# Kernel optimization log

Measured on AMD Instinct MI355X. Metric: run time of the kernel, lower is better.

Reference implementation:

```python
import jax, jax.numpy as jnp
import numpy as np

B, S, D = 8, 2048, 512

def setup_inputs() -> dict:
    key = jax.random.key(0)
    ks = jax.random.split(key, 9)
    scale = 1.0 / np.sqrt(D)
    q = jax.random.normal(ks[0], (B, S, D), dtype=jnp.float32)
    k = jax.random.normal(ks[1], (B, S, D), dtype=jnp.float32)
    v = jax.random.normal(ks[2], (B, S, D), dtype=jnp.float32)
    # causal mask, broadcast over batch: True = attend
    mask = jnp.tril(jnp.ones((S, S), dtype=bool))[None, :, :]
    Wq = jax.random.normal(ks[3], (D, D), dtype=jnp.float32) * scale
    bq = jax.random.normal(ks[4], (D,), dtype=jnp.float32) * scale
    Wk = jax.random.normal(ks[5], (D, D), dtype=jnp.float32) * scale
    bk = jax.random.normal(ks[6], (D,), dtype=jnp.float32) * scale
    Wv = jax.random.normal(ks[7], (D, D), dtype=jnp.float32) * scale
    bv = jax.random.normal(ks[8], (D,), dtype=jnp.float32) * scale
    return {"q": q, "k": k, "v": v, "mask": mask,
            "Wq": Wq, "bq": bq, "Wk": Wk, "bk": bk, "Wv": Wv, "bv": bv}

def reference(q, k, v, mask, Wq, bq, Wk, bk, Wv, bv):
    # torch nn.Linear: x @ W^T + b
    Q = jnp.einsum('bsd,ed->bse', q, Wq) + bq
    K = jnp.einsum('bsd,ed->bse', k, Wk) + bk
    V = jnp.einsum('bsd,ed->bse', v, Wv) + bv
    scores = jnp.einsum('bqd,bkd->bqk', Q, K) / jnp.sqrt(jnp.float32(D))
    scores = jnp.where(mask, scores, jnp.float32(-1e9))
    prob = jax.nn.softmax(scores, axis=-1)
    out = jnp.einsum('bqk,bkd->bqd', prob, V)
    return out
```

## Files before the change

### kernel.cpp

```cpp
#include <hip/hip_runtime.h>
#include <stdint.h>
#include <stddef.h>
#include <math.h>

typedef _Float16 half8 __attribute__((ext_vector_type(8)));
typedef float f32x4 __attribute__((ext_vector_type(4)));

#define SCALE_QK 0.04419417382415922f

__device__ __forceinline__ void gload16(const void* g, void* lds) {
  __builtin_amdgcn_global_load_lds(
      (const __attribute__((address_space(1))) void*)g,
      (__attribute__((address_space(3))) void*)lds,
      16, 0, 0);
}

template<bool A_F32>
__device__ __forceinline__ void run_kloop(const void* Arow0, const _Float16* Brow0,
                                          int lda, int ldb, int kIters,
                                          _Float16* As0, _Float16* As1,
                                          _Float16* Bs0, _Float16* Bs1,
                                          f32x4 (&acc)[4][4])
{
  const int tid  = threadIdx.x;
  const int lane = tid & 63;
  const int w    = tid >> 6;
  const int wm   = w >> 1, wn = w & 1;
  const int srow = tid >> 3;
  const int sg   = tid & 7;
  const int swz  = sg ^ (srow & 7);
  const int fr   = lane & 15;
  const int fq   = lane >> 4;
  const int fx   = lane & 7;

  f32x4 preF[8];

  auto loadAreg = [&](int it) {
    const float* A = (const float*)Arow0;
    const int k0 = it * 64;
    #pragma unroll
    for (int i = 0; i < 4; ++i) {
      const float* src = A + (size_t)(i*32 + srow) * lda + (k0 + sg*8);
      preF[2*i]   = *(const f32x4*)src;
      preF[2*i+1] = *(const f32x4*)(src + 4);
    }
  };
  auto writeA = [&](_Float16* dst) {
    #pragma unroll
    for (int i = 0; i < 4; ++i) {
      f32x4 x = preF[2*i], y = preF[2*i+1];
      half8 h;
      h[0]=(_Float16)x[0]; h[1]=(_Float16)x[1]; h[2]=(_Float16)x[2]; h[3]=(_Float16)x[3];
      h[4]=(_Float16)y[0]; h[5]=(_Float16)y[1]; h[6]=(_Float16)y[2]; h[7]=(_Float16)y[3];
      *(half8*)(dst + (i*32 + srow)*64 + swz*8) = h;
    }
  };
  auto gloadA = [&](int it, _Float16* dst) {
    const _Float16* A = (const _Float16*)Arow0;
    const int k0 = it * 64;
    #pragma unroll
    for (int i = 0; i < 4; ++i)
      gload16(A + (size_t)(i*32 + srow) * lda + (k0 + swz*8), dst + i*2048 + w*512);
  };
  auto gloadB = [&](int it, _Float16* dst) {
    const int k0 = it * 64;
    #pragma unroll
    for (int i = 0; i < 4; ++i)
      gload16(Brow0 + (size_t)(i*32 + srow) * ldb + (k0 + swz*8), dst + i*2048 + w*512);
  };
  auto stage = [&](int it, _Float16* dA, _Float16* dB) {
    if constexpr (A_F32) loadAreg(it);
    else                 gloadA(it, dA);
    gloadB(it, dB);
  };
  auto compute = [&](const _Float16* cAs, const _Float16* cBs) {
    #pragma unroll
    for (int ks = 0; ks < 2; ++ks) {
      half8 av[4], bv[4];
      const int slot = (ks*4 + fq) ^ fx;
      #pragma unroll
      for (int i = 0; i < 4; ++i) {
        av[i] = *(const half8*)(cAs + (wm*64 + i*16 + fr)*64 + slot*8);
        bv[i] = *(const half8*)(cBs + (wn*64 + i*16 + fr)*64 + slot*8);
      }
      #pragma unroll
      for (int i = 0; i < 4; ++i) {
        #pragma unroll
        for (int j = 0; j < 4; ++j)
          acc[i][j] = __builtin_amdgcn_mfma_f32_16x16x32_f16(av[i], bv[j], acc[i][j], 0, 0, 0);
      }
    }
  };

  stage(0, As0, Bs0);
  if constexpr (A_F32) writeA(As0);
  __syncthreads();

  for (int it = 0; it < kIters; it += 2) {
    stage(it + 1, As1, Bs1);
    compute(As0, Bs0);
    if constexpr (A_F32) writeA(As1);
    __syncthreads();
    const bool more = (it + 2) < kIters;
    if (more) stage(it + 2, As0, Bs0);
    compute(As1, Bs1);
    if constexpr (A_F32) { if (more) writeA(As0); }
    __syncthreads();
  }
}

__global__ __launch_bounds__(256) void k_cvtw(const float* __restrict__ Wq,
                                              const float* __restrict__ Wk,
                                              const float* __restrict__ Wv,
                                              _Float16* __restrict__ Wb)
{
  const int t = blockIdx.x * 256 + threadIdx.x;
  const int base = t * 8;
  const int z = base >> 18;
  const int off = base & 262143;
  const float* src = (z == 0) ? Wq : ((z == 1) ? Wk : Wv);
  f32x4 a = *(const f32x4*)(src + off);
  f32x4 b = *(const f32x4*)(src + off + 4);
  half8 h;
  h[0]=(_Float16)a[0]; h[1]=(_Float16)a[1]; h[2]=(_Float16)a[2]; h[3]=(_Float16)a[3];
  h[4]=(_Float16)b[0]; h[5]=(_Float16)b[1]; h[6]=(_Float16)b[2]; h[7]=(_Float16)b[3];
  *(half8*)(Wb + base) = h;
}

__global__ __launch_bounds__(256) void k_proj(const float* __restrict__ q,
                                              const float* __restrict__ k,
                                              const float* __restrict__ v,
                                              const _Float16* __restrict__ Wb,
                                              const float* __restrict__ bq,
                                              const float* __restrict__ bk,
                                              const float* __restrict__ bv,
                                              _Float16* __restrict__ Qb,
                                              _Float16* __restrict__ Kb,
                                              _Float16* __restrict__ Vb)
{
  __shared__ __align__(16) _Float16 As0[128*64], As1[128*64];
  __shared__ __align__(16) _Float16 Bs0[128*64], Bs1[128*64];
  const int bid = blockIdx.x;
  const int xcd = bid & 7, i = bid >> 3;
  const int p = xcd * 48 + (i >> 2);
  const int nt = i & 3;
  const int z = p >> 7, mt = p & 127;

  const float* A     = (z == 0) ? q  : (z == 1) ? k  : v;
  const float* bia   = (z == 0) ? bq : (z == 1) ? bk : bv;
  const _Float16* B  = Wb + (size_t)z * 512 * 512;
  _Float16* C        = (z == 0) ? Qb : (z == 1) ? Kb : Vb;

  f32x4 acc[4][4] = {};
  run_kloop<true>(A + (size_t)mt*128*512, B + (size_t)nt*128*512, 512, 512, 8,
                  As0, As1, Bs0, Bs1, acc);

  const int lane = threadIdx.x & 63, w = threadIdx.x >> 6;
  const int wm = w >> 1, wn = w & 1;
  const int fr = lane & 15, fq = lane >> 4;
  #pragma unroll
  for (int j = 0; j < 4; ++j) {
    const int col = nt*128 + wn*64 + j*16 + fr;
    const float bval = bia[col];
    #pragma unroll
    for (int i2 = 0; i2 < 4; ++i2) {
      const int row = mt*128 + wm*64 + i2*16 + fq*4;
      #pragma unroll
      for (int r = 0; r < 4; ++r)
        C[(size_t)(row + r) * 512 + col] = (_Float16)(acc[i2][j][r] + bval);
    }
  }
}

__global__ __launch_bounds__(256) void k_trans(const _Float16* __restrict__ Vb,
                                               _Float16* __restrict__ Vt)
{
  __shared__ __align__(16) _Float16 t[64][72];
  const int st = blockIdx.x, dt = blockIdx.y, b = blockIdx.z;
  const int r = threadIdx.x >> 2, g = threadIdx.x & 3;
  const _Float16* src = Vb + ((size_t)b*2048 + st*64 + r)*512 + dt*64 + g*16;
  half8 v0 = *(const half8*)src;
  half8 v1 = *(const half8*)(src + 8);
  *(half8*)&t[r][g*16]     = v0;
  *(half8*)&t[r][g*16 + 8] = v1;
  __syncthreads();
  half8 o0, o1;
  #pragma unroll
  for (int i2 = 0; i2 < 8; ++i2) o0[i2] = t[g*16 + i2][r];
  #pragma unroll
  for (int i2 = 0; i2 < 8; ++i2) o1[i2] = t[g*16 + 8 + i2][r];
  _Float16* dst = Vt + ((size_t)b*512 + dt*64 + r)*2048 + st*64 + g*16;
  *(half8*)dst       = o0;
  *(half8*)(dst + 8) = o1;
}

__global__ __launch_bounds__(256) void k_scores(const _Float16* __restrict__ Qb,
                                                const _Float16* __restrict__ Kb,
                                                _Float16* __restrict__ P)
{
  const int bid = blockIdx.x;
  const int b = bid & 7;
  const int t = bid >> 3;
  int qt = (int)((sqrtf(8.0f * (float)t + 1.0f) - 1.0f) * 0.5f);
  int base = (qt * (qt + 1)) >> 1;
  if (t < base)                { --qt; base = (qt * (qt + 1)) >> 1; }
  else if (t >= base + qt + 1) { ++qt; base = (qt * (qt + 1)) >> 1; }
  const int kt = t - base;

  __shared__ __align__(16) _Float16 As0[128*64], As1[128*64];
  __shared__ __align__(16) _Float16 Bs0[128*64], Bs1[128*64];
  f32x4 acc[4][4] = {};
  run_kloop<false>(Qb + ((size_t)b*2048 + qt*128)*512,
                   Kb + ((size_t)b*2048 + kt*128)*512,
                   512, 512, 8, As0, As1, Bs0, Bs1, acc);
  const int lane = threadIdx.x & 63, w = threadIdx.x >> 6;
  const int wm = w >> 1, wn = w & 1;
  const int fr = lane & 15, fq = lane >> 4;
  #pragma unroll
  for (int i = 0; i < 4; ++i) {
    const int row = qt*128 + wm*64 + i*16 + fq*4;
    #pragma unroll
    for (int j = 0; j < 4; ++j) {
      const int col = kt*128 + wn*64 + j*16 + fr;
      #pragma unroll
      for (int r = 0; r < 4; ++r)
        P[((size_t)b*2048 + row + r) * 2048 + col] = (_Float16)(acc[i][j][r] * SCALE_QK);
    }
  }
}

__global__ __launch_bounds__(256) void k_softmax(_Float16* __restrict__ P)
{
  const int lane = threadIdx.x & 63;
  const int row  = blockIdx.x * 4 + (threadIdx.x >> 6);
  const int qIdx = row & 2047;
  _Float16* p = P + (size_t)row * 2048;
  const int L    = qIdx + 1;
  const int Lpad = ((qIdx >> 7) + 1) * 128;

  half8 xb[4];
  float m = -1e30f, s = 0.f;
  #pragma unroll
  for (int c = 0; c < 4; ++c) {
    const int i0 = lane * 8 + c * 512;
    if (i0 < Lpad) {
      half8 x = *(const half8*)(p + i0);
      xb[c] = x;
      float xv[8];
      #pragma unroll
      for (int j = 0; j < 8; ++j) xv[j] = (i0 + j < L) ? (float)x[j] : -1e30f;
      float cm = xv[0];
      #pragma unroll
      for (int j = 1; j < 8; ++j) cm = fmaxf(cm, xv[j]);
      const float mn = fmaxf(m, cm);
      float cs = 0.f;
      #pragma unroll
      for (int j = 0; j < 8; ++j) cs += __expf(xv[j] - mn);
      s = s * __expf(m - mn) + cs;
      m = mn;
    }
  }
  #pragma unroll
  for (int d = 1; d < 64; d <<= 1) {
    const float mo = __shfl_xor(m, d, 64);
    const float so = __shfl_xor(s, d, 64);
    const float mn = fmaxf(m, mo);
    s = s * __expf(m - mn) + so * __expf(mo - mn);
    m = mn;
  }
  const float inv = 1.0f / s;

  #pragma unroll
  for (int c = 0; c < 4; ++c) {
    const int i0 = lane * 8 + c * 512;
    if (i0 < Lpad) {
      half8 x = xb[c];
      half8 o;
      #pragma unroll
      for (int j = 0; j < 8; ++j)
        o[j] = (i0 + j < L) ? (_Float16)(__expf((float)x[j] - m) * inv) : (_Float16)0.f;
      *(half8*)(p + i0) = o;
    }
  }
}

__global__ __launch_bounds__(256) void k_pv(const _Float16* __restrict__ P,
                                            const _Float16* __restrict__ Vt,
                                            float* __restrict__ Out)
{
  const int bid = blockIdx.x;
  const int b = bid & 7;
  const int r0 = bid >> 3;
  const int qi = r0 >> 2, dt = r0 & 3;
  const int qt = (qi & 1) ? (15 - (qi >> 1)) : (qi >> 1);

  __shared__ __align__(16) _Float16 As0[128*64], As1[128*64];
  __shared__ __align__(16) _Float16 Bs0[128*64], Bs1[128*64];
  f32x4 acc[4][4] = {};
  run_kloop<false>(P  + ((size_t)b*2048 + qt*128)*2048,
                   Vt + ((size_t)b*512  + dt*128)*2048,
                   2048, 2048, (qt + 1) * 2, As0, As1, Bs0, Bs1, acc);
  const int lane = threadIdx.x & 63, w = threadIdx.x >> 6;
  const int wm = w >> 1, wn = w & 1;
  const int fr = lane & 15, fq = lane >> 4;
  #pragma unroll
  for (int i = 0; i < 4; ++i) {
    const int row = qt*128 + wm*64 + i*16 + fq*4;
    #pragma unroll
    for (int j = 0; j < 4; ++j) {
      const int col = dt*128 + wn*64 + j*16 + fr;
      #pragma unroll
      for (int r = 0; r < 4; ++r)
        Out[((size_t)b*2048 + row + r) * 512 + col] = acc[i][j][r];
    }
  }
}

extern "C" void kernel_launch(void* const* d_in, const int* in_sizes, int n_in,
                              void* d_out, int out_size, void* d_ws, size_t ws_size,
                              hipStream_t stream) {
  (void)in_sizes; (void)n_in; (void)out_size;
  const float* q  = (const float*)d_in[0];
  const float* k  = (const float*)d_in[1];
  const float* v  = (const float*)d_in[2];
  const float* Wq = (const float*)d_in[4];
  const float* bq = (const float*)d_in[5];
  const float* Wk = (const float*)d_in[6];
  const float* bk = (const float*)d_in[7];
  const float* Wv = (const float*)d_in[8];
  const float* bv = (const float*)d_in[9];

  const size_t OFF_P  = 0;
  const size_t OFF_Q  = (size_t)64 << 20;
  const size_t OFF_K  = (size_t)80 << 20;
  const size_t OFF_V  = (size_t)96 << 20;
  const size_t OFF_VT = (size_t)112 << 20;
  const size_t OFF_W  = (size_t)128 << 20;
  const size_t NEEDED = OFF_W + (size_t)3 * 512 * 512 * sizeof(_Float16);
  if (ws_size < NEEDED) return;

  char* ws = (char*)d_ws;
  _Float16* P  = (_Float16*)(ws + OFF_P);
  _Float16* Qb = (_Float16*)(ws + OFF_Q);
  _Float16* Kb = (_Float16*)(ws + OFF_K);
  _Float16* Vb = (_Float16*)(ws + OFF_V);
  _Float16* Vt = (_Float16*)(ws + OFF_VT);
  _Float16* Wb = (_Float16*)(ws + OFF_W);
  float* Out = (float*)d_out;

  k_cvtw   <<<dim3(384),      dim3(256), 0, stream>>>(Wq, Wk, Wv, Wb);
  k_proj   <<<dim3(1536),     dim3(256), 0, stream>>>(q, k, v, Wb, bq, bk, bv, Qb, Kb, Vb);
  k_trans  <<<dim3(32, 8, 8), dim3(256), 0, stream>>>(Vb, Vt);
  k_scores <<<dim3(1088),     dim3(256), 0, stream>>>(Qb, Kb, P);
  k_softmax<<<dim3(4096),     dim3(256), 0, stream>>>(P);
  k_pv     <<<dim3(512),      dim3(256), 0, stream>>>(P, Vt, Out);
}
```

Before: 272.5 us.

## Single-buffer GEMM LDS for higher occupancy and fuse V transpose into projection

Replaces the double-buffered LDS k-loop with a single-buffered load-sync-compute loop, halving LDS per block. Launch bounds now request 3-4 blocks per CU to raise occupancy. The V projection writes its transposed tile through LDS straight into Vt, so the separate transpose kernel and Vb round trip are removed. The trade-off is that global loads no longer overlap MFMA compute within a block, so latency hiding now relies on other resident blocks.

After: 262.7 us. 1.04x faster.

```diff
diff --git a/kernel.cpp b/kernel.cpp
--- a/kernel.cpp
+++ b/kernel.cpp
@@ -16,11 +16,10 @@
 }
 
 template<bool A_F32>
-__device__ __forceinline__ void run_kloop(const void* Arow0, const _Float16* Brow0,
-                                          int lda, int ldb, int kIters,
-                                          _Float16* As0, _Float16* As1,
-                                          _Float16* Bs0, _Float16* Bs1,
-                                          f32x4 (&acc)[4][4])
+__device__ __forceinline__ void run_kloop_sb(const void* Arow0, const _Float16* Brow0,
+                                             int lda, int ldb, int kIters,
+                                             _Float16* As, _Float16* Bs,
+                                             f32x4 (&acc)[4][4])
 {
   const int tid  = threadIdx.x;
   const int lane = tid & 63;
@@ -33,55 +32,47 @@
   const int fq   = lane >> 4;
   const int fx   = lane & 7;
 
-  f32x4 preF[8];
-
-  auto loadAreg = [&](int it) {
-    const float* A = (const float*)Arow0;
+  for (int it = 0; it < kIters; ++it) {
     const int k0 = it * 64;
-    #pragma unroll
-    for (int i = 0; i < 4; ++i) {
-      const float* src = A + (size_t)(i*32 + srow) * lda + (k0 + sg*8);
-      preF[2*i]   = *(const f32x4*)src;
-      preF[2*i+1] = *(const f32x4*)(src + 4);
-    }
-  };
-  auto writeA = [&](_Float16* dst) {
-    #pragma unroll
-    for (int i = 0; i < 4; ++i) {
-      f32x4 x = preF[2*i], y = preF[2*i+1];
-      half8 h;
-      h[0]=(_Float16)x[0]; h[1]=(_Float16)x[1]; h[2]=(_Float16)x[2]; h[3]=(_Float16)x[3];
-      h[4]=(_Float16)y[0]; h[5]=(_Float16)y[1]; h[6]=(_Float16)y[2]; h[7]=(_Float16)y[3];
-      *(half8*)(dst + (i*32 + srow)*64 + swz*8) = h;
-    }
-  };
-  auto gloadA = [&](int it, _Float16* dst) {
-    const _Float16* A = (const _Float16*)Arow0;
-    const int k0 = it * 64;
-    #pragma unroll
-    for (int i = 0; i < 4; ++i)
-      gload16(A + (size_t)(i*32 + srow) * lda + (k0 + swz*8), dst + i*2048 + w*512);
-  };
-  auto gloadB = [&](int it, _Float16* dst) {
-    const int k0 = it * 64;
-    #pragma unroll
-    for (int i = 0; i < 4; ++i)
-      gload16(Brow0 + (size_t)(i*32 + srow) * ldb + (k0 + swz*8), dst + i*2048 + w*512);
-  };
-  auto stage = [&](int it, _Float16* dA, _Float16* dB) {
-    if constexpr (A_F32) loadAreg(it);
-    else                 gloadA(it, dA);
-    gloadB(it, dB);
-  };
-  auto compute = [&](const _Float16* cAs, const _Float16* cBs) {
+    if constexpr (A_F32) {
+      const float* A = (const float*)Arow0;
+      f32x4 preF[8];
+      #pragma unroll
+      for (int i = 0; i < 4; ++i) {
+        const float* src = A + (size_t)(i*32 + srow) * lda + (k0 + sg*8);
+        preF[2*i]   = *(const f32x4*)src;
+        preF[2*i+1] = *(const f32x4*)(src + 4);
+      }
+      #pragma unroll
+      for (int i = 0; i < 4; ++i)
+        gload16(Brow0 + (size_t)(i*32 + srow) * ldb + (k0 + swz*8), Bs + i*2048 + w*512);
+      #pragma unroll
+      for (int i = 0; i < 4; ++i) {
+        f32x4 x = preF[2*i], y = preF[2*i+1];
+        half8 h;
+        h[0]=(_Float16)x[0]; h[1]=(_Float16)x[1]; h[2]=(_Float16)x[2]; h[3]=(_Float16)x[3];
+        h[4]=(_Float16)y[0]; h[5]=(_Float16)y[1]; h[6]=(_Float16)y[2]; h[7]=(_Float16)y[3];
+        *(half8*)(As + (i*32 + srow)*64 + swz*8) = h;
+      }
+    } else {
+      const _Float16* A = (const _Float16*)Arow0;
+      #pragma unroll
+      for (int i = 0; i < 4; ++i)
+        gload16(A + (size_t)(i*32 + srow) * lda + (k0 + swz*8), As + i*2048 + w*512);
+      #pragma unroll
+      for (int i = 0; i < 4; ++i)
+        gload16(Brow0 + (size_t)(i*32 + srow) * ldb + (k0 + swz*8), Bs + i*2048 + w*512);
+    }
+    __syncthreads();
+
     #pragma unroll
     for (int ks = 0; ks < 2; ++ks) {
       half8 av[4], bv[4];
       const int slot = (ks*4 + fq) ^ fx;
       #pragma unroll
       for (int i = 0; i < 4; ++i) {
-        av[i] = *(const half8*)(cAs + (wm*64 + i*16 + fr)*64 + slot*8);
-        bv[i] = *(const half8*)(cBs + (wn*64 + i*16 + fr)*64 + slot*8);
+        av[i] = *(const half8*)(As + (wm*64 + i*16 + fr)*64 + slot*8);
+        bv[i] = *(const half8*)(Bs + (wn*64 + i*16 + fr)*64 + slot*8);
       }
       #pragma unroll
       for (int i = 0; i < 4; ++i) {
@@ -90,21 +81,6 @@
           acc[i][j] = __builtin_amdgcn_mfma_f32_16x16x32_f16(av[i], bv[j], acc[i][j], 0, 0, 0);
       }
     }
-  };
-
-  stage(0, As0, Bs0);
-  if constexpr (A_F32) writeA(As0);
-  __syncthreads();
-
-  for (int it = 0; it < kIters; it += 2) {
-    stage(it + 1, As1, Bs1);
-    compute(As0, Bs0);
-    if constexpr (A_F32) writeA(As1);
-    __syncthreads();
-    const bool more = (it + 2) < kIters;
-    if (more) stage(it + 2, As0, Bs0);
-    compute(As1, Bs1);
-    if constexpr (A_F32) { if (more) writeA(As0); }
     __syncthreads();
   }
 }
@@ -127,19 +103,21 @@
   *(half8*)(Wb + base) = h;
 }
 
-__global__ __launch_bounds__(256) void k_proj(const float* __restrict__ q,
-                                              const float* __restrict__ k,
-                                              const float* __restrict__ v,
-                                              const _Float16* __restrict__ Wb,
-                                              const float* __restrict__ bq,
-                                              const float* __restrict__ bk,
-                                              const float* __restrict__ bv,
-                                              _Float16* __restrict__ Qb,
-                                              _Float16* __restrict__ Kb,
-                                              _Float16* __restrict__ Vb)
-{
-  __shared__ __align__(16) _Float16 As0[128*64], As1[128*64];
-  __shared__ __align__(16) _Float16 Bs0[128*64], Bs1[128*64];
+__global__ __launch_bounds__(256, 3) void k_proj(const float* __restrict__ q,
+                                                 const float* __restrict__ k,
+                                                 const float* __restrict__ v,
+                                                 const _Float16* __restrict__ Wb,
+                                                 const float* __restrict__ bq,
+                                                 const float* __restrict__ bk,
+                                                 const float* __restrict__ bv,
+                                                 _Float16* __restrict__ Qb,
+                                                 _Float16* __restrict__ Kb,
+                                                 _Float16* __restrict__ Vt)
+{
+  __shared__ __align__(16) _Float16 LDSbuf[128*132];
+  _Float16* As = LDSbuf;
+  _Float16* Bs = LDSbuf + 8192;
+
   const int bid = blockIdx.x;
   const int xcd = bid & 7, i = bid >> 3;
   const int p = xcd * 48 + (i >> 2);
@@ -149,55 +127,61 @@
   const float* A     = (z == 0) ? q  : (z == 1) ? k  : v;
   const float* bia   = (z == 0) ? bq : (z == 1) ? bk : bv;
   const _Float16* B  = Wb + (size_t)z * 512 * 512;
-  _Float16* C        = (z == 0) ? Qb : (z == 1) ? Kb : Vb;
 
   f32x4 acc[4][4] = {};
-  run_kloop<true>(A + (size_t)mt*128*512, B + (size_t)nt*128*512, 512, 512, 8,
-                  As0, As1, Bs0, Bs1, acc);
-
-  const int lane = threadIdx.x & 63, w = threadIdx.x >> 6;
+  run_kloop_sb<true>(A + (size_t)mt*128*512, B + (size_t)nt*128*512, 512, 512, 8,
+                     As, Bs, acc);
+
+  const int tid = threadIdx.x;
+  const int lane = tid & 63, w = tid >> 6;
   const int wm = w >> 1, wn = w & 1;
   const int fr = lane & 15, fq = lane >> 4;
-  #pragma unroll
-  for (int j = 0; j < 4; ++j) {
-    const int col = nt*128 + wn*64 + j*16 + fr;
-    const float bval = bia[col];
-    #pragma unroll
-    for (int i2 = 0; i2 < 4; ++i2) {
-      const int row = mt*128 + wm*64 + i2*16 + fq*4;
-      #pragma unroll
-      for (int r = 0; r < 4; ++r)
-        C[(size_t)(row + r) * 512 + col] = (_Float16)(acc[i2][j][r] + bval);
-    }
-  }
-}
-
-__global__ __launch_bounds__(256) void k_trans(const _Float16* __restrict__ Vb,
-                                               _Float16* __restrict__ Vt)
-{
-  __shared__ __align__(16) _Float16 t[64][72];
-  const int st = blockIdx.x, dt = blockIdx.y, b = blockIdx.z;
-  const int r = threadIdx.x >> 2, g = threadIdx.x & 3;
-  const _Float16* src = Vb + ((size_t)b*2048 + st*64 + r)*512 + dt*64 + g*16;
-  half8 v0 = *(const half8*)src;
-  half8 v1 = *(const half8*)(src + 8);
-  *(half8*)&t[r][g*16]     = v0;
-  *(half8*)&t[r][g*16 + 8] = v1;
-  __syncthreads();
-  half8 o0, o1;
-  #pragma unroll
-  for (int i2 = 0; i2 < 8; ++i2) o0[i2] = t[g*16 + i2][r];
-  #pragma unroll
-  for (int i2 = 0; i2 < 8; ++i2) o1[i2] = t[g*16 + 8 + i2][r];
-  _Float16* dst = Vt + ((size_t)b*512 + dt*64 + r)*2048 + st*64 + g*16;
-  *(half8*)dst       = o0;
-  *(half8*)(dst + 8) = o1;
-}
-
-__global__ __launch_bounds__(256) void k_scores(const _Float16* __restrict__ Qb,
-                                                const _Float16* __restrict__ Kb,
-                                                _Float16* __restrict__ P)
-{
+
+  if (z < 2) {
+    _Float16* C = (z == 0) ? Qb : Kb;
+    #pragma unroll
+    for (int j = 0; j < 4; ++j) {
+      const int col = nt*128 + wn*64 + j*16 + fr;
+      const float bval = bia[col];
+      #pragma unroll
+      for (int i2 = 0; i2 < 4; ++i2) {
+        const int row = mt*128 + wm*64 + i2*16 + fq*4;
+        #pragma unroll
+        for (int r = 0; r < 4; ++r)
+          C[(size_t)(row + r) * 512 + col] = (_Float16)(acc[i2][j][r] + bval);
+      }
+    }
+  } else {
+    _Float16* sm = LDSbuf;
+    #pragma unroll
+    for (int j = 0; j < 4; ++j) {
+      const int colloc = wn*64 + j*16 + fr;
+      const float bval = bia[nt*128 + colloc];
+      #pragma unroll
+      for (int i2 = 0; i2 < 4; ++i2) {
+        const int rowloc = wm*64 + i2*16 + fq*4;
+        #pragma unroll
+        for (int r = 0; r < 4; ++r)
+          sm[colloc*132 + rowloc + r] = (_Float16)(acc[i2][j][r] + bval);
+      }
+    }
+    __syncthreads();
+    const int bb = mt >> 4, s0 = (mt & 15) * 128;
+    #pragma unroll
+    for (int q8 = 0; q8 < 8; ++q8) {
+      const int dloc = q8*16 + (tid >> 4);
+      const int ch   = tid & 15;
+      half8 o = *(const half8*)&sm[dloc*132 + ch*8];
+      *(half8*)(Vt + ((size_t)bb*512 + nt*128 + dloc)*2048 + s0 + ch*8) = o;
+    }
+  }
+}
+
+__global__ __launch_bounds__(256, 4) void k_scores(const _Float16* __restrict__ Qb,
+                                                   const _Float16* __restrict__ Kb,
+                                                   _Float16* __restrict__ P)
+{
+  __shared__ __align__(16) _Float16 As[128*64], Bs[128*64];
   const int bid = blockIdx.x;
   const int b = bid & 7;
   const int t = bid >> 3;
@@ -207,12 +191,10 @@
   else if (t >= base + qt + 1) { ++qt; base = (qt * (qt + 1)) >> 1; }
   const int kt = t - base;
 
-  __shared__ __align__(16) _Float16 As0[128*64], As1[128*64];
-  __shared__ __align__(16) _Float16 Bs0[128*64], Bs1[128*64];
   f32x4 acc[4][4] = {};
-  run_kloop<false>(Qb + ((size_t)b*2048 + qt*128)*512,
-                   Kb + ((size_t)b*2048 + kt*128)*512,
-                   512, 512, 8, As0, As1, Bs0, Bs1, acc);
+  run_kloop_sb<false>(Qb + ((size_t)b*2048 + qt*128)*512,
+                      Kb + ((size_t)b*2048 + kt*128)*512,
+                      512, 512, 8, As, Bs, acc);
   const int lane = threadIdx.x & 63, w = threadIdx.x >> 6;
   const int wm = w >> 1, wn = w & 1;
   const int fr = lane & 15, fq = lane >> 4;
@@ -284,22 +266,21 @@
   }
 }
 
-__global__ __launch_bounds__(256) void k_pv(const _Float16* __restrict__ P,
-                                            const _Float16* __restrict__ Vt,
-                                            float* __restrict__ Out)
-{
+__global__ __launch_bounds__(256, 4) void k_pv(const _Float16* __restrict__ P,
+                                               const _Float16* __restrict__ Vt,
+                                               float* __restrict__ Out)
+{
+  __shared__ __align__(16) _Float16 As[128*64], Bs[128*64];
   const int bid = blockIdx.x;
   const int b = bid & 7;
   const int r0 = bid >> 3;
   const int qi = r0 >> 2, dt = r0 & 3;
   const int qt = (qi & 1) ? (15 - (qi >> 1)) : (qi >> 1);
 
-  __shared__ __align__(16) _Float16 As0[128*64], As1[128*64];
-  __shared__ __align__(16) _Float16 Bs0[128*64], Bs1[128*64];
   f32x4 acc[4][4] = {};
-  run_kloop<false>(P  + ((size_t)b*2048 + qt*128)*2048,
-                   Vt + ((size_t)b*512  + dt*128)*2048,
-                   2048, 2048, (qt + 1) * 2, As0, As1, Bs0, Bs1, acc);
+  run_kloop_sb<false>(P  + ((size_t)b*2048 + qt*128)*2048,
+                      Vt + ((size_t)b*512  + dt*128)*2048,
+                      2048, 2048, (qt + 1) * 2, As, Bs, acc);
   const int lane = threadIdx.x & 63, w = threadIdx.x >> 6;
   const int wm = w >> 1, wn = w & 1;
   const int fr = lane & 15, fq = lane >> 4;
@@ -333,7 +314,6 @@
   const size_t OFF_P  = 0;
   const size_t OFF_Q  = (size_t)64 << 20;
   const size_t OFF_K  = (size_t)80 << 20;
-  const size_t OFF_V  = (size_t)96 << 20;
   const size_t OFF_VT = (size_t)112 << 20;
   const size_t OFF_W  = (size_t)128 << 20;
   const size_t NEEDED = OFF_W + (size_t)3 * 512 * 512 * sizeof(_Float16);
@@ -343,15 +323,13 @@
   _Float16* P  = (_Float16*)(ws + OFF_P);
   _Float16* Qb = (_Float16*)(ws + OFF_Q);
   _Float16* Kb = (_Float16*)(ws + OFF_K);
-  _Float16* Vb = (_Float16*)(ws + OFF_V);
   _Float16* Vt = (_Float16*)(ws + OFF_VT);
   _Float16* Wb = (_Float16*)(ws + OFF_W);
   float* Out = (float*)d_out;
 
-  k_cvtw   <<<dim3(384),      dim3(256), 0, stream>>>(Wq, Wk, Wv, Wb);
-  k_proj   <<<dim3(1536),     dim3(256), 0, stream>>>(q, k, v, Wb, bq, bk, bv, Qb, Kb, Vb);
-  k_trans  <<<dim3(32, 8, 8), dim3(256), 0, stream>>>(Vb, Vt);
-  k_scores <<<dim3(1088),     dim3(256), 0, stream>>>(Qb, Kb, P);
-  k_softmax<<<dim3(4096),     dim3(256), 0, stream>>>(P);
-  k_pv     <<<dim3(512),      dim3(256), 0, stream>>>(P, Vt, Out);
-}
+  k_cvtw   <<<dim3(384),  dim3(256), 0, stream>>>(Wq, Wk, Wv, Wb);
+  k_proj   <<<dim3(1536), dim3(256), 0, stream>>>(q, k, v, Wb, bq, bk, bv, Qb, Kb, Vt);
+  k_scores <<<dim3(1088), dim3(256), 0, stream>>>(Qb, Kb, P);
+  k_softmax<<<dim3(4096), dim3(256), 0, stream>>>(P);
+  k_pv     <<<dim3(512),  dim3(256), 0, stream>>>(P, Vt, Out);
+}
```
